# Kernel optimization log

Hardware: AMD Instinct MI355X
Metric: run time of the kernel (lower is better)

## Reference

```python
import jax, jax.numpy as jnp
import numpy as np

B, H, W, C = 4, 256, 256, 96
WIN = 8            # window size
HEADS = 3
HD = C // HEADS    # head dim = 32
SCALE = HD ** -0.5
N = WIN * WIN      # tokens per window = 64
HID = 4 * C        # MLP hidden


def _rel_pos_index(w):
    coords = np.stack(np.meshgrid(np.arange(w), np.arange(w), indexing='ij')).reshape(2, -1)
    rel = coords[:, :, None] - coords[:, None, :]         # (2, N, N)
    rel = rel.transpose(1, 2, 0).astype(np.int64)          # (N, N, 2)
    rel[:, :, 0] += w - 1
    rel[:, :, 1] += w - 1
    rel[:, :, 0] *= 2 * w - 1
    return jnp.asarray(rel.sum(-1))                        # (N, N)

REL_IDX = _rel_pos_index(WIN)


def layernorm(x, g, b, eps=1e-5):
    mu = jnp.mean(x, -1, keepdims=True)
    var = jnp.mean(jnp.square(x - mu), -1, keepdims=True)
    return (x - mu) * jax.lax.rsqrt(var + eps) * g + b


def setup_inputs() -> dict:
    key = jax.random.key(0)
    ks = jax.random.split(key, 8)
    s = 0.02
    return {
        'x': jax.random.normal(ks[0], (B, H, W, C), jnp.float32),
        'norm1_g': jnp.ones((C,), jnp.float32),
        'norm1_b': jnp.zeros((C,), jnp.float32),
        'qkv_w': jax.random.normal(ks[1], (C, 3 * C), jnp.float32) * s,
        'qkv_b': jnp.zeros((3 * C,), jnp.float32),
        'proj_w': jax.random.normal(ks[2], (C, C), jnp.float32) * s,
        'proj_b': jnp.zeros((C,), jnp.float32),
        'rel_bias_table': jax.random.normal(ks[3], ((2 * WIN - 1) ** 2, HEADS), jnp.float32) * s,
        'norm2_g': jnp.ones((C,), jnp.float32),
        'norm2_b': jnp.zeros((C,), jnp.float32),
        'fc1_w': jax.random.normal(ks[4], (C, HID), jnp.float32) * s,
        'fc1_b': jnp.zeros((HID,), jnp.float32),
        'fc2_w': jax.random.normal(ks[5], (HID, C), jnp.float32) * s,
        'fc2_b': jnp.zeros((C,), jnp.float32),
    }


def reference(x, norm1_g, norm1_b, qkv_w, qkv_b, proj_w, proj_b,
              rel_bias_table, norm2_g, norm2_b, fc1_w, fc1_b, fc2_w, fc2_b):
    shortcut = x
    h = layernorm(x, norm1_g, norm1_b)
    # window partition: (B,H,W,C) -> (B*nW, N, C)
    hw = h.reshape(B, H // WIN, WIN, W // WIN, WIN, C)
    hw = hw.transpose(0, 1, 3, 2, 4, 5).reshape(-1, N, C)
    Bw = hw.shape[0]
    # qkv projection
    qkv = hw @ qkv_w + qkv_b                               # (Bw, N, 3C)
    qkv = qkv.reshape(Bw, N, 3, HEADS, HD)
    q = jnp.transpose(qkv[:, :, 0], (0, 2, 1, 3))          # (Bw, h, N, d)
    k = jnp.transpose(qkv[:, :, 1], (0, 2, 1, 3))
    v = jnp.transpose(qkv[:, :, 2], (0, 2, 1, 3))
    attn = jnp.einsum('bhnd,bhmd->bhnm', q * SCALE, k)     # (Bw, h, N, N)
    bias = rel_bias_table[REL_IDX].transpose(2, 0, 1)      # (h, N, N)
    attn = jax.nn.softmax(attn + bias[None], axis=-1)
    out = jnp.einsum('bhnm,bhmd->bhnd', attn, v)
    out = out.transpose(0, 2, 1, 3).reshape(Bw, N, C)
    out = out @ proj_w + proj_b
    # window reverse: (B*nW, N, C) -> (B,H,W,C)
    out = out.reshape(B, H // WIN, W // WIN, WIN, WIN, C)
    out = out.transpose(0, 1, 3, 2, 4, 5).reshape(B, H, W, C)
    x = shortcut + out
    h2 = layernorm(x, norm2_g, norm2_b)
    mlp = jax.nn.gelu(h2 @ fc1_w + fc1_b, approximate=False) @ fc2_w + fc2_b
    return x + mlp
```

## Files before the change

kernel.cpp:

```cpp
#include <hip/hip_runtime.h>
#include <hip/hip_bf16.h>

#define NWIN 4096
#define SCALE 0.17677669529663687f

typedef __attribute__((ext_vector_type(8))) short bf16x8;
typedef __attribute__((ext_vector_type(4))) float f32x4;

__device__ __forceinline__ unsigned short f2bf(float f) {
    __hip_bfloat16 h = __float2bfloat16(f);
    return *reinterpret_cast<unsigned short*>(&h);
}
__device__ __forceinline__ f32x4 MF(bf16x8 a, bf16x8 b, f32x4 c) {
    return __builtin_amdgcn_mfma_f32_16x16x32_bf16(a, b, c, 0, 0, 0);
}
__device__ __forceinline__ bf16x8 LD8(const unsigned short* p) {
    return *reinterpret_cast<const bf16x8*>(p);
}

__global__ __launch_bounds__(512) void k_prep(
    const float* __restrict__ qkvw, const float* __restrict__ projw,
    const float* __restrict__ fc1w, const float* __restrict__ fc2w,
    unsigned short* __restrict__ ws)
{
    int i = blockIdx.x*512 + threadIdx.x;
    if (i >= 110592) return;
    float v;
    if (i < 27648)      { int j = i;        int n = j/96,  k = j%96;  v = qkvw[k*288 + n]; }
    else if (i < 36864) { int j = i-27648;  int n = j/96,  k = j%96;  v = projw[k*96 + n]; }
    else if (i < 73728) { int j = i-36864;  int n = j/96,  k = j%96;  v = fc1w[k*384 + n]; }
    else                { int j = i-73728;  int n = j/384, k = j%384; v = fc2w[k*96 + n]; }
    ws[i] = f2bf(v);
}

__global__ __launch_bounds__(512) void k_fused(
    const float* __restrict__ x,
    const float* __restrict__ n1g, const float* __restrict__ n1b,
    const float* __restrict__ qkv_b, const float* __restrict__ proj_b,
    const float* __restrict__ btab,
    const float* __restrict__ n2g, const float* __restrict__ n2b,
    const float* __restrict__ fc1b, const float* __restrict__ fc2b,
    const unsigned short* __restrict__ wbf, float* __restrict__ out)
{
    extern __shared__ char smem[];
    float*          s_res  = (float*)smem;
    unsigned short* s_a    = (unsigned short*)(smem + 25600);
    unsigned short* s_w    = (unsigned short*)(smem + 38912);
    float*          s_bias = (float*)(smem + 58880);
    float*          s_s    = (float*)(smem + 61584);
    unsigned short* s_p    = (unsigned short*)(smem + 78480);
    unsigned short* s_w2   = (unsigned short*)(smem + 78848);
    unsigned short* s_q    = (unsigned short*)(smem + 117248);
    unsigned short* s_k    = (unsigned short*)(smem + 132608);
    unsigned short* s_vt   = (unsigned short*)(smem + 147968);
    unsigned short* s_h    = (unsigned short*)(smem + 117248);

    const int tid  = threadIdx.x;
    const int wid  = tid >> 6, lane = tid & 63, l16 = lane & 15, l4 = lane >> 4;
    const int wb   = blockIdx.x;
    const int b    = wb >> 10, wrem = wb & 1023, wy = wrem >> 5, wx = wrem & 31;
    const long base = ((long)(b*256 + wy*8)*256 + (long)(wx*8))*96;
    const int mtile = wid >> 1;
    const int nh    = wid & 1;

    for (int i = tid; i < 64*24; i += 512) {
        int tok = i / 24, seg = i % 24;
        const float4 v = *reinterpret_cast<const float4*>(
            x + base + (long)(((tok >> 3) << 8) + (tok & 7))*96 + seg*4);
        *reinterpret_cast<float4*>(s_res + tok*100 + seg*4) = v;
    }
    __syncthreads();

    {
        const int tok = tid >> 3, part = tid & 7;
        float r[12]; float s1 = 0.f, s2 = 0.f;
        #pragma unroll
        for (int i = 0; i < 12; ++i) { float v = s_res[tok*100 + part*12 + i]; r[i]=v; s1+=v; s2+=v*v; }
        s1 += __shfl_xor(s1,1); s2 += __shfl_xor(s2,1);
        s1 += __shfl_xor(s1,2); s2 += __shfl_xor(s2,2);
        s1 += __shfl_xor(s1,4); s2 += __shfl_xor(s2,4);
        float mu = s1*(1.f/96.f), var = s2*(1.f/96.f) - mu*mu;
        float rs = rsqrtf(var + 1e-5f);
        #pragma unroll
        for (int i = 0; i < 12; ++i) {
            int c = part*12 + i;
            s_a[tok*104 + c] = f2bf((r[i]-mu)*rs*n1g[c] + n1b[c]);
        }
    }
    {
        uint4* dst = reinterpret_cast<uint4*>(s_w);
        const uint4* src = reinterpret_cast<const uint4*>(wbf);
        for (int i = tid; i < 288*12; i += 512) {
            int r = i / 12, sg = i % 12;
            dst[r*13 + sg] = src[r*12 + sg];
        }
    }
    __syncthreads();

    {
        const unsigned short* ap = s_a + (mtile*16 + l16)*104 + l4*8;
        const bf16x8 a0 = LD8(ap), a1 = LD8(ap+32), a2 = LD8(ap+64);
        #pragma unroll
        for (int u = 0; u < 9; ++u) {
            const int ntile = nh*9 + u;
            const unsigned short* bp = s_w + (ntile*16 + l16)*104 + l4*8;
            f32x4 acc = {0.f,0.f,0.f,0.f};
            acc = MF(a0, LD8(bp),    acc);
            acc = MF(a1, LD8(bp+32), acc);
            acc = MF(a2, LD8(bp+64), acc);
            const int col = ntile*16 + l16;
            const float bv = qkv_b[col];
            const int sel = col/96, hc = col%96, h = hc >> 5, d = hc & 31;
            if (sel < 2) {
                unsigned short* q = (sel == 0 ? s_q : s_k) + h*2560 + d;
                #pragma unroll
                for (int r = 0; r < 4; ++r)
                    q[(mtile*16 + l4*4 + r)*40] = f2bf(acc[r] + bv);
            } else {
                unsigned short* q = s_vt + h*2304 + d*72 + mtile*16 + l4*4;
                #pragma unroll
                for (int r = 0; r < 4; ++r)
                    q[r] = f2bf(acc[r] + bv);
            }
        }
    }
    __syncthreads();

    for (int h = 0; h < 3; ++h) {
        {
            const unsigned short* ap = s_q + h*2560 + (mtile*16 + l16)*40 + l4*8;
            const bf16x8 af = LD8(ap);
            #pragma unroll
            for (int u = 0; u < 2; ++u) {
                const int ntile = nh*2 + u;
                const unsigned short* bp = s_k + h*2560 + (ntile*16 + l16)*40 + l4*8;
                f32x4 acc = {0.f,0.f,0.f,0.f};
                acc = MF(af, LD8(bp), acc);
                #pragma unroll
                for (int r = 0; r < 4; ++r)
                    s_s[(mtile*16 + l4*4 + r)*66 + ntile*16 + l16] = acc[r];
            }
        }
        if (h == 0) {
            uint4* dst = reinterpret_cast<uint4*>(s_w);
            const uint4* src = reinterpret_cast<const uint4*>(wbf) + 3456;
            for (int i = tid; i < 96*12; i += 512) {
                int r = i/12, sg = i%12;
                dst[r*13 + sg] = src[r*12 + sg];
            }
            for (int i = tid; i < 675; i += 512) s_bias[i] = btab[i];
        }
        __syncthreads();
        {
            const int i = tid >> 3, part = tid & 7;
            const int yi = i >> 3, xi = i & 7;
            float v[8]; float m = -1e30f;
            #pragma unroll
            for (int u = 0; u < 8; ++u) {
                int j = part*8 + u, yj = j >> 3, xj = j & 7;
                int ridx = (yi-yj+7)*15 + (xi-xj+7);
                v[u] = s_s[i*66 + j]*SCALE + s_bias[ridx*3 + h];
                m = fmaxf(m, v[u]);
            }
            m = fmaxf(m, __shfl_xor(m,1)); m = fmaxf(m, __shfl_xor(m,2)); m = fmaxf(m, __shfl_xor(m,4));
            float s = 0.f;
            #pragma unroll
            for (int u = 0; u < 8; ++u) { v[u] = __expf(v[u] - m); s += v[u]; }
            s += __shfl_xor(s,1); s += __shfl_xor(s,2); s += __shfl_xor(s,4);
            const float inv = 1.f/s;
            #pragma unroll
            for (int u = 0; u < 8; ++u) s_p[i*72 + part*8 + u] = f2bf(v[u]*inv);
        }
        __syncthreads();
        {
            const unsigned short* ap = s_p + (mtile*16 + l16)*72 + l4*8;
            const bf16x8 a0 = LD8(ap), a1 = LD8(ap+32);
            const unsigned short* bp = s_vt + h*2304 + (nh*16 + l16)*72 + l4*8;
            f32x4 acc = {0.f,0.f,0.f,0.f};
            acc = MF(a0, LD8(bp),    acc);
            acc = MF(a1, LD8(bp+32), acc);
            #pragma unroll
            for (int r = 0; r < 4; ++r)
                s_a[(mtile*16 + l4*4 + r)*104 + h*32 + nh*16 + l16] = f2bf(acc[r]);
        }
        __syncthreads();
    }

    {
        const unsigned short* ap = s_a + (mtile*16 + l16)*104 + l4*8;
        const bf16x8 a0 = LD8(ap), a1 = LD8(ap+32), a2 = LD8(ap+64);
        #pragma unroll
        for (int u = 0; u < 3; ++u) {
            const int ntile = nh*3 + u;
            const unsigned short* bp = s_w + (ntile*16 + l16)*104 + l4*8;
            f32x4 acc = {0.f,0.f,0.f,0.f};
            acc = MF(a0, LD8(bp),    acc);
            acc = MF(a1, LD8(bp+32), acc);
            acc = MF(a2, LD8(bp+64), acc);
            const int c = ntile*16 + l16;
            const float pb = proj_b[c];
            #pragma unroll
            for (int r = 0; r < 4; ++r) {
                const int tok = mtile*16 + l4*4 + r;
                s_res[tok*100 + c] += acc[r] + pb;
            }
        }
    }
    __syncthreads();

    {
        const int tok = tid >> 3, part = tid & 7;
        float r[12]; float s1 = 0.f, s2 = 0.f;
        #pragma unroll
        for (int i = 0; i < 12; ++i) { float v = s_res[tok*100 + part*12 + i]; r[i]=v; s1+=v; s2+=v*v; }
        s1 += __shfl_xor(s1,1); s2 += __shfl_xor(s2,1);
        s1 += __shfl_xor(s1,2); s2 += __shfl_xor(s2,2);
        s1 += __shfl_xor(s1,4); s2 += __shfl_xor(s2,4);
        float mu = s1*(1.f/96.f), var = s2*(1.f/96.f) - mu*mu;
        float rs = rsqrtf(var + 1e-5f);
        #pragma unroll
        for (int i = 0; i < 12; ++i) {
            int c = part*12 + i;
            s_a[tok*104 + c] = f2bf((r[i]-mu)*rs*n2g[c] + n2b[c]);
        }
    }
    f32x4 macc[3];
    #pragma unroll
    for (int u = 0; u < 3; ++u) macc[u] = (f32x4){0.f,0.f,0.f,0.f};

    for (int ch = 0; ch < 2; ++ch) {
        if (ch) __syncthreads();
        {
            uint4* d1 = reinterpret_cast<uint4*>(s_w);
            uint4* d2 = reinterpret_cast<uint4*>(s_w2);
            const uint4* src = reinterpret_cast<const uint4*>(wbf);
            for (int i = tid; i < 192*12; i += 512) {
                int r = i/12, sg = i%12;
                d1[r*13 + sg] = src[4608 + (ch*192 + r)*12 + sg];
            }
            for (int i = tid; i < 96*24; i += 512) {
                int n = i/24, sg = i%24;
                d2[n*25 + sg] = src[9216 + n*48 + ch*24 + sg];
            }
        }
        __syncthreads();
        {
            const unsigned short* ap = s_a + (mtile*16 + l16)*104 + l4*8;
            const bf16x8 a0 = LD8(ap), a1 = LD8(ap+32), a2 = LD8(ap+64);
            #pragma unroll
            for (int u = 0; u < 6; ++u) {
                const int ntile = nh*6 + u;
                const unsigned short* bp = s_w + (ntile*16 + l16)*104 + l4*8;
                f32x4 acc = {0.f,0.f,0.f,0.f};
                acc = MF(a0, LD8(bp),    acc);
                acc = MF(a1, LD8(bp+32), acc);
                acc = MF(a2, LD8(bp+64), acc);
                const int hcol = ntile*16 + l16;
                const float fb = fc1b[ch*192 + hcol];
                #pragma unroll
                for (int r = 0; r < 4; ++r) {
                    float v = acc[r] + fb;
                    float g = 0.5f*v*(1.f + erff(v*0.70710678118654752f));
                    s_h[(mtile*16 + l4*4 + r)*200 + hcol] = f2bf(g);
                }
            }
        }
        __syncthreads();
        {
            const unsigned short* ap = s_h + (mtile*16 + l16)*200 + l4*8;
            bf16x8 af[6];
            #pragma unroll
            for (int kc = 0; kc < 6; ++kc) af[kc] = LD8(ap + kc*32);
            #pragma unroll
            for (int u = 0; u < 3; ++u) {
                const unsigned short* bp = s_w2 + ((nh*3 + u)*16 + l16)*200 + l4*8;
                #pragma unroll
                for (int kc = 0; kc < 6; ++kc)
                    macc[u] = MF(af[kc], LD8(bp + kc*32), macc[u]);
            }
        }
    }

    {
        #pragma unroll
        for (int u = 0; u < 3; ++u) {
            const int c = (nh*3 + u)*16 + l16;
            const float fb = fc2b[c];
            #pragma unroll
            for (int r = 0; r < 4; ++r) {
                const int tok = mtile*16 + l4*4 + r;
                out[base + (long)(((tok >> 3) << 8) + (tok & 7))*96 + c] =
                    s_res[tok*100 + c] + macc[u][r] + fb;
            }
        }
    }
}

extern "C" void kernel_launch(void* const* d_in, const int* in_sizes, int n_in,
                              void* d_out, int out_size, void* d_ws, size_t ws_size,
                              hipStream_t stream) {
    (void)in_sizes; (void)n_in; (void)out_size; (void)ws_size;
    const float* x     = (const float*)d_in[0];
    const float* n1g   = (const float*)d_in[1];
    const float* n1b   = (const float*)d_in[2];
    const float* qkvw  = (const float*)d_in[3];
    const float* qkvb  = (const float*)d_in[4];
    const float* projw = (const float*)d_in[5];
    const float* projb = (const float*)d_in[6];
    const float* btab  = (const float*)d_in[7];
    const float* n2g   = (const float*)d_in[8];
    const float* n2b   = (const float*)d_in[9];
    const float* fc1w  = (const float*)d_in[10];
    const float* fc1b  = (const float*)d_in[11];
    const float* fc2w  = (const float*)d_in[12];
    const float* fc2b  = (const float*)d_in[13];
    float* out = (float*)d_out;
    unsigned short* ws = (unsigned short*)d_ws;

    hipFuncSetAttribute(reinterpret_cast<const void*>(k_fused),
                        hipFuncAttributeMaxDynamicSharedMemorySize, 161792);

    k_prep<<<dim3(216), dim3(512), 0, stream>>>(qkvw, projw, fc1w, fc2w, ws);
    k_fused<<<dim3(NWIN), dim3(512), 161792, stream>>>(
        x, n1g, n1b, qkvb, projb, btab, n2g, n2b, fc1b, fc2b, ws, out);
}
```

Before: 483.9 us.

## Read MFMA weights from global memory directly and pipeline attention heads

Weight staging into shared memory is dropped, and all MFMA B operands now read the pre-transposed bf16 weights straight from global memory (L2/L1 cached). This cuts LDS use from about 158KB to about 110KB and removes several barriers. The scale and relative-position bias are folded into the QK^T store. The PV matmul of the previous head is overlapped with the QK of the next head, which saves one sync per head. The erf GELU is replaced by a tanh-approximation sigmoid form, a numerical change from the exact reference, and shared-memory accesses are vectorised. The prep kernel now writes transposed output with coalesced reads.

```diff
diff --git a/kernel.cpp b/kernel.cpp
--- a/kernel.cpp
+++ b/kernel.cpp
@@ -6,6 +6,8 @@
 
 typedef __attribute__((ext_vector_type(8))) short bf16x8;
 typedef __attribute__((ext_vector_type(4))) float f32x4;
+typedef __attribute__((ext_vector_type(4))) unsigned short u16x4;
+typedef __attribute__((ext_vector_type(8))) unsigned short u16x8;
 
 __device__ __forceinline__ unsigned short f2bf(float f) {
     __hip_bfloat16 h = __float2bfloat16(f);
@@ -25,12 +27,10 @@
 {
     int i = blockIdx.x*512 + threadIdx.x;
     if (i >= 110592) return;
-    float v;
-    if (i < 27648)      { int j = i;        int n = j/96,  k = j%96;  v = qkvw[k*288 + n]; }
-    else if (i < 36864) { int j = i-27648;  int n = j/96,  k = j%96;  v = projw[k*96 + n]; }
-    else if (i < 73728) { int j = i-36864;  int n = j/96,  k = j%96;  v = fc1w[k*384 + n]; }
-    else                { int j = i-73728;  int n = j/384, k = j%384; v = fc2w[k*96 + n]; }
-    ws[i] = f2bf(v);
+    if (i < 27648)      { int k = i/288,        n = i%288; ws[n*96 + k]         = f2bf(qkvw[i]); }
+    else if (i < 36864) { int j = i-27648;  int k = j/96,  n = j%96;  ws[27648 + n*96 + k]  = f2bf(projw[j]); }
+    else if (i < 73728) { int j = i-36864;  int k = j/384, n = j%384; ws[36864 + n*96 + k]  = f2bf(fc1w[j]); }
+    else                { int j = i-73728;  int k = j/96,  n = j%96;  ws[73728 + n*384 + k] = f2bf(fc2w[j]); }
 }
 
 __global__ __launch_bounds__(512) void k_fused(
@@ -45,15 +45,13 @@
     extern __shared__ char smem[];
     float*          s_res  = (float*)smem;
     unsigned short* s_a    = (unsigned short*)(smem + 25600);
-    unsigned short* s_w    = (unsigned short*)(smem + 38912);
-    float*          s_bias = (float*)(smem + 58880);
-    float*          s_s    = (float*)(smem + 61584);
-    unsigned short* s_p    = (unsigned short*)(smem + 78480);
-    unsigned short* s_w2   = (unsigned short*)(smem + 78848);
-    unsigned short* s_q    = (unsigned short*)(smem + 117248);
-    unsigned short* s_k    = (unsigned short*)(smem + 132608);
-    unsigned short* s_vt   = (unsigned short*)(smem + 147968);
-    unsigned short* s_h    = (unsigned short*)(smem + 117248);
+    float*          s_bias = (float*)(smem + 38912);
+    float*          s_s    = (float*)(smem + 41616);
+    unsigned short* s_p    = (unsigned short*)(smem + 59024);
+    unsigned short* s_q    = (unsigned short*)(smem + 68240);
+    unsigned short* s_k    = (unsigned short*)(smem + 83600);
+    unsigned short* s_vt   = (unsigned short*)(smem + 98960);
+    unsigned short* s_h    = (unsigned short*)(smem + 68240);
 
     const int tid  = threadIdx.x;
     const int wid  = tid >> 6, lane = tid & 63, l16 = lane & 15, l4 = lane >> 4;
@@ -69,30 +67,34 @@
             x + base + (long)(((tok >> 3) << 8) + (tok & 7))*96 + seg*4);
         *reinterpret_cast<float4*>(s_res + tok*100 + seg*4) = v;
     }
+    for (int i = tid; i < 675; i += 512) s_bias[i] = btab[i];
     __syncthreads();
 
     {
         const int tok = tid >> 3, part = tid & 7;
-        float r[12]; float s1 = 0.f, s2 = 0.f;
-        #pragma unroll
-        for (int i = 0; i < 12; ++i) { float v = s_res[tok*100 + part*12 + i]; r[i]=v; s1+=v; s2+=v*v; }
+        const float* rp = s_res + tok*100 + part*12;
+        float4 v0 = *reinterpret_cast<const float4*>(rp);
+        float4 v1 = *reinterpret_cast<const float4*>(rp + 4);
+        float4 v2 = *reinterpret_cast<const float4*>(rp + 8);
+        float r[12] = {v0.x,v0.y,v0.z,v0.w, v1.x,v1.y,v1.z,v1.w, v2.x,v2.y,v2.z,v2.w};
+        float s1 = 0.f, s2 = 0.f;
+        #pragma unroll
+        for (int i = 0; i < 12; ++i) { s1 += r[i]; s2 += r[i]*r[i]; }
         s1 += __shfl_xor(s1,1); s2 += __shfl_xor(s2,1);
         s1 += __shfl_xor(s1,2); s2 += __shfl_xor(s2,2);
         s1 += __shfl_xor(s1,4); s2 += __shfl_xor(s2,4);
         float mu = s1*(1.f/96.f), var = s2*(1.f/96.f) - mu*mu;
         float rs = rsqrtf(var + 1e-5f);
-        #pragma unroll
-        for (int i = 0; i < 12; ++i) {
-            int c = part*12 + i;
-            s_a[tok*104 + c] = f2bf((r[i]-mu)*rs*n1g[c] + n1b[c]);
-        }
-    }
-    {
-        uint4* dst = reinterpret_cast<uint4*>(s_w);
-        const uint4* src = reinterpret_cast<const uint4*>(wbf);
-        for (int i = tid; i < 288*12; i += 512) {
-            int r = i / 12, sg = i % 12;
-            dst[r*13 + sg] = src[r*12 + sg];
+        unsigned short* wp = s_a + tok*104 + part*12;
+        #pragma unroll
+        for (int q = 0; q < 3; ++q) {
+            u16x4 pk;
+            #pragma unroll
+            for (int j = 0; j < 4; ++j) {
+                int c = part*12 + q*4 + j;
+                pk[j] = f2bf((r[q*4+j]-mu)*rs*n1g[c] + n1b[c]);
+            }
+            *reinterpret_cast<u16x4*>(wp + q*4) = pk;
         }
     }
     __syncthreads();
@@ -103,7 +105,7 @@
         #pragma unroll
         for (int u = 0; u < 9; ++u) {
             const int ntile = nh*9 + u;
-            const unsigned short* bp = s_w + (ntile*16 + l16)*104 + l4*8;
+            const unsigned short* bp = wbf + (ntile*16 + l16)*96 + l4*8;
             f32x4 acc = {0.f,0.f,0.f,0.f};
             acc = MF(a0, LD8(bp),    acc);
             acc = MF(a1, LD8(bp+32), acc);
@@ -117,10 +119,10 @@
                 for (int r = 0; r < 4; ++r)
                     q[(mtile*16 + l4*4 + r)*40] = f2bf(acc[r] + bv);
             } else {
-                unsigned short* q = s_vt + h*2304 + d*72 + mtile*16 + l4*4;
-                #pragma unroll
-                for (int r = 0; r < 4; ++r)
-                    q[r] = f2bf(acc[r] + bv);
+                u16x4 pk;
+                #pragma unroll
+                for (int r = 0; r < 4; ++r) pk[r] = f2bf(acc[r] + bv);
+                *reinterpret_cast<u16x4*>(s_vt + h*2304 + d*72 + mtile*16 + l4*4) = pk;
             }
         }
     }
@@ -136,55 +138,63 @@
                 const unsigned short* bp = s_k + h*2560 + (ntile*16 + l16)*40 + l4*8;
                 f32x4 acc = {0.f,0.f,0.f,0.f};
                 acc = MF(af, LD8(bp), acc);
-                #pragma unroll
-                for (int r = 0; r < 4; ++r)
-                    s_s[(mtile*16 + l4*4 + r)*66 + ntile*16 + l16] = acc[r];
-            }
-        }
-        if (h == 0) {
-            uint4* dst = reinterpret_cast<uint4*>(s_w);
-            const uint4* src = reinterpret_cast<const uint4*>(wbf) + 3456;
-            for (int i = tid; i < 96*12; i += 512) {
-                int r = i/12, sg = i%12;
-                dst[r*13 + sg] = src[r*12 + sg];
-            }
-            for (int i = tid; i < 675; i += 512) s_bias[i] = btab[i];
+                const int col = ntile*16 + l16;
+                const int yj = col >> 3, xj = col & 7;
+                #pragma unroll
+                for (int r = 0; r < 4; ++r) {
+                    const int row = mtile*16 + l4*4 + r;
+                    const int yi = row >> 3, xi = row & 7;
+                    const int ridx = (yi-yj+7)*15 + (xi-xj+7);
+                    s_s[row*68 + col] = acc[r]*SCALE + s_bias[ridx*3 + h];
+                }
+            }
+        }
+        if (h > 0) {
+            const unsigned short* ap = s_p + (mtile*16 + l16)*72 + l4*8;
+            const bf16x8 a0 = LD8(ap), a1 = LD8(ap+32);
+            const unsigned short* bp = s_vt + (h-1)*2304 + (nh*16 + l16)*72 + l4*8;
+            f32x4 acc = {0.f,0.f,0.f,0.f};
+            acc = MF(a0, LD8(bp),    acc);
+            acc = MF(a1, LD8(bp+32), acc);
+            #pragma unroll
+            for (int r = 0; r < 4; ++r)
+                s_a[(mtile*16 + l4*4 + r)*104 + (h-1)*32 + nh*16 + l16] = f2bf(acc[r]);
         }
         __syncthreads();
         {
             const int i = tid >> 3, part = tid & 7;
-            const int yi = i >> 3, xi = i & 7;
-            float v[8]; float m = -1e30f;
-            #pragma unroll
-            for (int u = 0; u < 8; ++u) {
-                int j = part*8 + u, yj = j >> 3, xj = j & 7;
-                int ridx = (yi-yj+7)*15 + (xi-xj+7);
-                v[u] = s_s[i*66 + j]*SCALE + s_bias[ridx*3 + h];
-                m = fmaxf(m, v[u]);
-            }
+            const float* sp = s_s + i*68 + part*8;
+            float4 v0 = *reinterpret_cast<const float4*>(sp);
+            float4 v1 = *reinterpret_cast<const float4*>(sp + 4);
+            float v[8] = {v0.x,v0.y,v0.z,v0.w, v1.x,v1.y,v1.z,v1.w};
+            float m = v[0];
+            #pragma unroll
+            for (int u = 1; u < 8; ++u) m = fmaxf(m, v[u]);
             m = fmaxf(m, __shfl_xor(m,1)); m = fmaxf(m, __shfl_xor(m,2)); m = fmaxf(m, __shfl_xor(m,4));
             float s = 0.f;
             #pragma unroll
             for (int u = 0; u < 8; ++u) { v[u] = __expf(v[u] - m); s += v[u]; }
             s += __shfl_xor(s,1); s += __shfl_xor(s,2); s += __shfl_xor(s,4);
             const float inv = 1.f/s;
-            #pragma unroll
-            for (int u = 0; u < 8; ++u) s_p[i*72 + part*8 + u] = f2bf(v[u]*inv);
+            u16x8 pk;
+            #pragma unroll
+            for (int u = 0; u < 8; ++u) pk[u] = f2bf(v[u]*inv);
+            *reinterpret_cast<u16x8*>(s_p + i*72 + part*8) = pk;
         }
         __syncthreads();
-        {
-            const unsigned short* ap = s_p + (mtile*16 + l16)*72 + l4*8;
-            const bf16x8 a0 = LD8(ap), a1 = LD8(ap+32);
-            const unsigned short* bp = s_vt + h*2304 + (nh*16 + l16)*72 + l4*8;
-            f32x4 acc = {0.f,0.f,0.f,0.f};
-            acc = MF(a0, LD8(bp),    acc);
-            acc = MF(a1, LD8(bp+32), acc);
-            #pragma unroll
-            for (int r = 0; r < 4; ++r)
-                s_a[(mtile*16 + l4*4 + r)*104 + h*32 + nh*16 + l16] = f2bf(acc[r]);
-        }
-        __syncthreads();
-    }
+    }
+    {
+        const unsigned short* ap = s_p + (mtile*16 + l16)*72 + l4*8;
+        const bf16x8 a0 = LD8(ap), a1 = LD8(ap+32);
+        const unsigned short* bp = s_vt + 2*2304 + (nh*16 + l16)*72 + l4*8;
+        f32x4 acc = {0.f,0.f,0.f,0.f};
+        acc = MF(a0, LD8(bp),    acc);
+        acc = MF(a1, LD8(bp+32), acc);
+        #pragma unroll
+        for (int r = 0; r < 4; ++r)
+            s_a[(mtile*16 + l4*4 + r)*104 + 2*32 + nh*16 + l16] = f2bf(acc[r]);
+    }
+    __syncthreads();
 
     {
         const unsigned short* ap = s_a + (mtile*16 + l16)*104 + l4*8;
@@ -192,7 +202,7 @@
         #pragma unroll
         for (int u = 0; u < 3; ++u) {
             const int ntile = nh*3 + u;
-            const unsigned short* bp = s_w + (ntile*16 + l16)*104 + l4*8;
+            const unsigned short* bp = wbf + 27648 + (ntile*16 + l16)*96 + l4*8;
             f32x4 acc = {0.f,0.f,0.f,0.f};
             acc = MF(a0, LD8(bp),    acc);
             acc = MF(a1, LD8(bp+32), acc);
@@ -210,57 +220,55 @@
 
     {
         const int tok = tid >> 3, part = tid & 7;
-        float r[12]; float s1 = 0.f, s2 = 0.f;
-        #pragma unroll
-        for (int i = 0; i < 12; ++i) { float v = s_res[tok*100 + part*12 + i]; r[i]=v; s1+=v; s2+=v*v; }
+        const float* rp = s_res + tok*100 + part*12;
+        float4 v0 = *reinterpret_cast<const float4*>(rp);
+        float4 v1 = *reinterpret_cast<const float4*>(rp + 4);
+        float4 v2 = *reinterpret_cast<const float4*>(rp + 8);
+        float r[12] = {v0.x,v0.y,v0.z,v0.w, v1.x,v1.y,v1.z,v1.w, v2.x,v2.y,v2.z,v2.w};
+        float s1 = 0.f, s2 = 0.f;
+        #pragma unroll
+        for (int i = 0; i < 12; ++i) { s1 += r[i]; s2 += r[i]*r[i]; }
         s1 += __shfl_xor(s1,1); s2 += __shfl_xor(s2,1);
         s1 += __shfl_xor(s1,2); s2 += __shfl_xor(s2,2);
         s1 += __shfl_xor(s1,4); s2 += __shfl_xor(s2,4);
         float mu = s1*(1.f/96.f), var = s2*(1.f/96.f) - mu*mu;
         float rs = rsqrtf(var + 1e-5f);
-        #pragma unroll
-        for (int i = 0; i < 12; ++i) {
-            int c = part*12 + i;
-            s_a[tok*104 + c] = f2bf((r[i]-mu)*rs*n2g[c] + n2b[c]);
-        }
-    }
+        unsigned short* wp = s_a + tok*104 + part*12;
+        #pragma unroll
+        for (int q = 0; q < 3; ++q) {
+            u16x4 pk;
+            #pragma unroll
+            for (int j = 0; j < 4; ++j) {
+                int c = part*12 + q*4 + j;
+                pk[j] = f2bf((r[q*4+j]-mu)*rs*n2g[c] + n2b[c]);
+            }
+            *reinterpret_cast<u16x4*>(wp + q*4) = pk;
+        }
+    }
+    __syncthreads();
+
     f32x4 macc[3];
     #pragma unroll
     for (int u = 0; u < 3; ++u) macc[u] = (f32x4){0.f,0.f,0.f,0.f};
 
     for (int ch = 0; ch < 2; ++ch) {
-        if (ch) __syncthreads();
-        {
-            uint4* d1 = reinterpret_cast<uint4*>(s_w);
-            uint4* d2 = reinterpret_cast<uint4*>(s_w2);
-            const uint4* src = reinterpret_cast<const uint4*>(wbf);
-            for (int i = tid; i < 192*12; i += 512) {
-                int r = i/12, sg = i%12;
-                d1[r*13 + sg] = src[4608 + (ch*192 + r)*12 + sg];
-            }
-            for (int i = tid; i < 96*24; i += 512) {
-                int n = i/24, sg = i%24;
-                d2[n*25 + sg] = src[9216 + n*48 + ch*24 + sg];
-            }
-        }
-        __syncthreads();
         {
             const unsigned short* ap = s_a + (mtile*16 + l16)*104 + l4*8;
             const bf16x8 a0 = LD8(ap), a1 = LD8(ap+32), a2 = LD8(ap+64);
             #pragma unroll
             for (int u = 0; u < 6; ++u) {
                 const int ntile = nh*6 + u;
-                const unsigned short* bp = s_w + (ntile*16 + l16)*104 + l4*8;
+                const int hcol = ntile*16 + l16;
+                const unsigned short* bp = wbf + 36864 + (ch*192 + hcol)*96 + l4*8;
                 f32x4 acc = {0.f,0.f,0.f,0.f};
                 acc = MF(a0, LD8(bp),    acc);
                 acc = MF(a1, LD8(bp+32), acc);
                 acc = MF(a2, LD8(bp+64), acc);
-                const int hcol = ntile*16 + l16;
                 const float fb = fc1b[ch*192 + hcol];
                 #pragma unroll
                 for (int r = 0; r < 4; ++r) {
                     float v = acc[r] + fb;
-                    float g = 0.5f*v*(1.f + erff(v*0.70710678118654752f));
+                    float g = v / (1.f + __expf(-1.5957691216057308f*(v + 0.044715f*v*v*v)));
                     s_h[(mtile*16 + l4*4 + r)*200 + hcol] = f2bf(g);
                 }
             }
@@ -273,12 +281,14 @@
             for (int kc = 0; kc < 6; ++kc) af[kc] = LD8(ap + kc*32);
             #pragma unroll
             for (int u = 0; u < 3; ++u) {
-                const unsigned short* bp = s_w2 + ((nh*3 + u)*16 + l16)*200 + l4*8;
+                const int n = (nh*3 + u)*16 + l16;
+                const unsigned short* bp = wbf + 73728 + n*384 + ch*192 + l4*8;
                 #pragma unroll
                 for (int kc = 0; kc < 6; ++kc)
                     macc[u] = MF(af[kc], LD8(bp + kc*32), macc[u]);
             }
         }
+        if (ch == 0) __syncthreads();
     }
 
     {
@@ -318,9 +328,9 @@
     unsigned short* ws = (unsigned short*)d_ws;
 
     hipFuncSetAttribute(reinterpret_cast<const void*>(k_fused),
-                        hipFuncAttributeMaxDynamicSharedMemorySize, 161792);
+                        hipFuncAttributeMaxDynamicSharedMemorySize, 112784);
 
     k_prep<<<dim3(216), dim3(512), 0, stream>>>(qkvw, projw, fc1w, fc2w, ws);
-    k_fused<<<dim3(NWIN), dim3(512), 161792, stream>>>(
+    k_fused<<<dim3(NWIN), dim3(512), 112784, stream>>>(
         x, n1g, n1b, qkvb, projb, btab, n2g, n2b, fc1b, fc2b, ws, out);
 }
```

Result: slower. 595.6 us (+23.1%).
